# Performance work log

Measured on AMD Instinct MI355X. Metric: run time of the kernel, lower is better.

The kernel has to match this reference:

```python
import jax, jax.numpy as jnp
import numpy as np

B, S, D, E, H, K = 64, 2048, 1024, 32, 4096, 8


def setup_inputs() -> dict:
    key = jax.random.key(0)
    k0, k1, k2, k3 = jax.random.split(key, 4)
    x = jax.random.normal(k0, (B, S, D), jnp.float32)
    # gate: nn.Linear(D, E) -> weight [E, D], bias [E]
    gate_w = jax.random.normal(k1, (E, D), jnp.float32) * (1.0 / np.sqrt(D))
    gate_b = jnp.zeros((E,), jnp.float32)
    # expert weights include the bias row (input dim + 1)
    w1 = jax.random.normal(k2, (E, D + 1, H), jnp.float32) * (1.0 / np.sqrt(D + 1))
    w2 = jax.random.normal(k3, (E, H + 1, D), jnp.float32) * (1.0 / np.sqrt(H + 1))
    return {"x": x, "gate_w": gate_w, "gate_b": gate_b, "w1": w1, "w2": w2}


def reference(x, gate_w, gate_b, w1, w2):
    b, s, d = x.shape
    # gating: softmax over the TOKEN axis (expert-choice routing)
    logits = jnp.einsum('bsd,ed->bse', x, gate_w) + gate_b          # [b, s, E]
    probs = jax.nn.softmax(logits, axis=-2)                          # softmax over tokens
    # top-k tokens per expert (torch.topk over dim=-2)
    vals_t, idx_t = jax.lax.top_k(probs.transpose(0, 2, 1), K)      # [b, E, k]
    vals = vals_t.transpose(0, 2, 1)                                 # [b, k, E]
    idx = idx_t.transpose(0, 2, 1)                                   # [b, k, E]
    flat_idx = idx.reshape(b, K * E)                                 # gather order: [k, E] flattened
    # gather selected tokens
    tok = jnp.take_along_axis(x, flat_idx[:, :, None], axis=1)       # [b, k*E, d]
    tok = tok.reshape(b, K, E, d)
    # weighted merge (mux) of the k tokens per expert
    merged = jnp.einsum('bked,bke->bed', tok, vals)                  # [b, E, d]
    ones = jnp.ones(merged.shape[:-1] + (1,), merged.dtype)
    # expert FFN (bias folded into the extra weight row)
    h = jnp.einsum('bei,eih->beh', jnp.concatenate([merged, ones], -1), w1)
    h = jax.nn.gelu(h, approximate=False)                            # torch nn.GELU() = exact erf
    o = jnp.einsum('bej,ejo->beo', jnp.concatenate([h, ones], -1), w2)  # [b, E, d]
    # demux: broadcast expert output back to its k tokens, weighted, scatter-add
    out_tok = jnp.einsum('beo,bke->bkeo', o, vals).reshape(b, K * E, d)
    out = jnp.zeros_like(x).at[jnp.arange(b)[:, None], flat_idx].add(out_tok)
    return out
```

## Files before the change

kernel.cpp:

```cpp
#include <hip/hip_runtime.h>
#include <hip/hip_bf16.h>
#include <math.h>

constexpr int NB = 64;
constexpr int NS = 2048;
constexpr int ND = 1024;
constexpr int NE = 32;
constexpr int NH = 4096;
constexpr int NK = 8;

typedef short bf16x8 __attribute__((ext_vector_type(8)));
typedef float f32x4  __attribute__((ext_vector_type(4)));

__device__ __forceinline__ unsigned short f2bf_rne(float v) {
  unsigned u = __builtin_bit_cast(unsigned, v);
  u += 0x7fffu + ((u >> 16) & 1u);
  return (unsigned short)(u >> 16);
}

__device__ __forceinline__ void gload_lds16(const void* g, void* l) {
  __builtin_amdgcn_global_load_lds(
      (const __attribute__((address_space(1))) unsigned*)g,
      (__attribute__((address_space(3))) unsigned*)l, 16, 0, 0);
}

__global__ __launch_bounds__(256) void k_gate_mfma(const float* __restrict__ x,
                                                   const float* __restrict__ gw,
                                                   float* __restrict__ logitsT) {
  const int b  = blockIdx.y;
  const int s0 = blockIdx.x * 128;
  const int t  = threadIdx.x;
  const int l  = t & 63;
  const int w  = t >> 6;

  __shared__ char smem[40960];
  float* trans = (float*)smem;

  f32x4 acc[2][2] = {};

  const int xr_ = t >> 4, xc = (t & 15) * 4;
  const int ge = t >> 3,  gk = (t & 7) * 8;

  float xreg[8][4];
  float wreg[8];

  auto issue = [&](int kt) {
    const int k0 = kt * 64;
#pragma unroll
    for (int p = 0; p < 8; ++p) {
      const int r = p * 16 + xr_;
      *(float4*)xreg[p] = *(const float4*)&x[((size_t)b * NS + s0 + r) * ND + k0 + xc];
    }
    *(float4*)&wreg[0] = *(const float4*)&gw[(size_t)ge * ND + k0 + gk];
    *(float4*)&wreg[4] = *(const float4*)&gw[(size_t)ge * ND + k0 + gk + 4];
  };
  auto commit = [&](int dst) {
    short* Ah = (short*)(smem + dst * 16384);
    short* Bh = (short*)(smem + 32768 + dst * 4096);
#pragma unroll
    for (int p = 0; p < 8; ++p) {
      const int r = p * 16 + xr_;
      unsigned short h[4];
#pragma unroll
      for (int j = 0; j < 4; ++j) h[j] = f2bf_rne(xreg[p][j]);
      const int off = r * 64 + (xc ^ ((r & 7) * 8));
      *(ushort4*)&Ah[off] = *(const ushort4*)h;
    }
    unsigned short h8[8];
#pragma unroll
    for (int j = 0; j < 8; ++j) h8[j] = f2bf_rne(wreg[j]);
    const int boff = ge * 64 + (gk ^ ((ge & 7) * 8));
    *(uint4*)&Bh[boff] = *(const uint4*)h8;
  };
  auto mfma_phase = [&](int cur) {
    const short* Ah = (const short*)(smem + cur * 16384);
    const short* Bh = (const short*)(smem + 32768 + cur * 4096);
#pragma unroll
    for (int ks = 0; ks < 2; ++ks) {
      const int koff = ks * 32 + (l >> 4) * 8;
      bf16x8 a[2], bb[2];
#pragma unroll
      for (int mf = 0; mf < 2; ++mf) {
        const int r = w * 32 + mf * 16 + (l & 15);
        a[mf] = *(const bf16x8*)&Ah[r * 64 + (koff ^ ((r & 7) * 8))];
      }
#pragma unroll
      for (int nf = 0; nf < 2; ++nf) {
        const int n = nf * 16 + (l & 15);
        bb[nf] = *(const bf16x8*)&Bh[n * 64 + (koff ^ ((n & 7) * 8))];
      }
#pragma unroll
      for (int mf = 0; mf < 2; ++mf)
#pragma unroll
        for (int nf = 0; nf < 2; ++nf)
          acc[mf][nf] = __builtin_amdgcn_mfma_f32_16x16x32_bf16(a[mf], bb[nf], acc[mf][nf], 0, 0, 0);
    }
  };

  issue(0);
  commit(0);
  __syncthreads();
  int cur = 0;
  for (int kt = 0; kt < ND / 64; ++kt) {
    const bool more = (kt + 1 < ND / 64);
    if (more) issue(kt + 1);
    mfma_phase(cur);
    if (more) commit(cur ^ 1);
    __syncthreads();
    cur ^= 1;
  }

#pragma unroll
  for (int mf = 0; mf < 2; ++mf)
#pragma unroll
    for (int nf = 0; nf < 2; ++nf)
#pragma unroll
      for (int j = 0; j < 4; ++j) {
        const int sl = w * 32 + mf * 16 + (l >> 4) * 4 + j;
        const int ec = nf * 16 + (l & 15);
        trans[sl * 33 + ec] = acc[mf][nf][j];
      }
  __syncthreads();
  const int eo = t >> 3, sc = (t & 7) * 16;
#pragma unroll
  for (int j4 = 0; j4 < 4; ++j4) {
    float4 v;
    v.x = trans[(sc + j4 * 4 + 0) * 33 + eo];
    v.y = trans[(sc + j4 * 4 + 1) * 33 + eo];
    v.z = trans[(sc + j4 * 4 + 2) * 33 + eo];
    v.w = trans[(sc + j4 * 4 + 3) * 33 + eo];
    *(float4*)&logitsT[((size_t)b * NE + eo) * NS + s0 + sc + j4 * 4] = v;
  }
}

__global__ __launch_bounds__(256) void k_topk(const float* __restrict__ logitsT,
                                              const float* __restrict__ x,
                                              const float* __restrict__ gw,
                                              float* __restrict__ tval,
                                              int* __restrict__ tidx) {
  const int be = blockIdx.x, b = be >> 5, e = be & 31;
  const float* row = logitsT + (size_t)be * NS;
  const int t = threadIdx.x, w = t >> 6, lane = t & 63;

  __shared__ float  cv[64];
  __shared__ int    cix[64];
  __shared__ double wsum[4];
  __shared__ float  smax;
  __shared__ int    gci[16];
  __shared__ float  glc[16];
  __shared__ double ginv;

  float v[8]; int si[8];
#pragma unroll
  for (int j = 0; j < 8; ++j) {
    const int s = w * 512 + lane + j * 64;
    v[j] = row[s]; si[j] = s;
  }
#pragma unroll
  for (int i = 0; i < 7; ++i)
#pragma unroll
    for (int j = 0; j < 7 - i; ++j) {
      const bool sw = (v[j + 1] > v[j]) || (v[j + 1] == v[j] && si[j + 1] < si[j]);
      const float tv = sw ? v[j + 1] : v[j];
      const int   ti = sw ? si[j + 1] : si[j];
      v[j + 1] = sw ? v[j] : v[j + 1];  si[j + 1] = sw ? si[j] : si[j + 1];
      v[j] = tv;  si[j] = ti;
    }
  const float mxl = v[0];
  double s8 = 1.0;
#pragma unroll
  for (int j = 1; j < 8; ++j) s8 += (double)expf(v[j] - mxl);

  for (int r = 0; r < 16; ++r) {
    float bp = v[0]; int bi = si[0]; int bl = lane;
#pragma unroll
    for (int off = 1; off < 64; off <<= 1) {
      const float op = __shfl_xor(bp, off);
      const int   oi = __shfl_xor(bi, off);
      const int   ol = __shfl_xor(bl, off);
      if (op > bp || (op == bp && oi < bi)) { bp = op; bi = oi; bl = ol; }
    }
    if (lane == 0) { cv[w * 16 + r] = bp; cix[w * 16 + r] = bi; }
    if (lane == bl) {
      v[0]=v[1]; v[1]=v[2]; v[2]=v[3]; v[3]=v[4]; v[4]=v[5]; v[5]=v[6]; v[6]=v[7]; v[7]=-INFINITY;
      si[0]=si[1]; si[1]=si[2]; si[2]=si[3]; si[3]=si[4]; si[4]=si[5]; si[5]=si[6]; si[6]=si[7]; si[7]=0x7fffffff;
    }
  }
  __syncthreads();
  if (w == 0) {
    float mv = cv[lane]; int mi = cix[lane];
    for (int r = 0; r < 16; ++r) {
      float bp = mv; int bi = mi; int bl = lane;
#pragma unroll
      for (int off = 1; off < 64; off <<= 1) {
        const float op = __shfl_xor(bp, off);
        const int   oi = __shfl_xor(bi, off);
        const int   ol = __shfl_xor(bl, off);
        if (op > bp || (op == bp && oi < bi)) { bp = op; bi = oi; bl = ol; }
      }
      if (lane == 0) { gci[r] = bi; if (r == 0) smax = bp; }
      if (lane == bl) { mv = -INFINITY; mi = 0x7fffffff; }
    }
  }
  __syncthreads();
  const float mx = smax;
  double lsum = s8 * (double)expf(mxl - mx);
#pragma unroll
  for (int off = 32; off; off >>= 1) lsum += __shfl_xor(lsum, off);
  if (lane == 0) wsum[w] = lsum;
  __syncthreads();
  if (t == 0) ginv = 1.0 / (wsum[0] + wsum[1] + wsum[2] + wsum[3]);

  const int kb = lane * 16;
  float gwl[16];
  *(float4*)&gwl[0]  = *(const float4*)&gw[(size_t)e * ND + kb];
  *(float4*)&gwl[4]  = *(const float4*)&gw[(size_t)e * ND + kb + 4];
  *(float4*)&gwl[8]  = *(const float4*)&gw[(size_t)e * ND + kb + 8];
  *(float4*)&gwl[12] = *(const float4*)&gw[(size_t)e * ND + kb + 12];
#pragma unroll
  for (int q = 0; q < 4; ++q) {
    const int c = w * 4 + q;
    const int ciq = gci[c];
    const float* xr = x + ((size_t)b * NS + ciq) * ND + kb;
    float xv[16];
    *(float4*)&xv[0]  = *(const float4*)&xr[0];
    *(float4*)&xv[4]  = *(const float4*)&xr[4];
    *(float4*)&xv[8]  = *(const float4*)&xr[8];
    *(float4*)&xv[12] = *(const float4*)&xr[12];
    double d = 0.0;
#pragma unroll
    for (int j2 = 0; j2 < 16; ++j2) d += (double)xv[j2] * (double)gwl[j2];
#pragma unroll
    for (int off = 32; off; off >>= 1) d += __shfl_xor(d, off);
    if (lane == 0) glc[c] = (float)d;
  }
  __syncthreads();
  if (t < 16) {
    const float mylc = glc[t]; const int myci = gci[t];
    int rank = 0;
#pragma unroll
    for (int c2 = 0; c2 < 16; ++c2) {
      if (c2 == t) continue;
      rank += (glc[c2] > mylc) || (glc[c2] == mylc && gci[c2] < myci);
    }
    if (rank < 8) {
      tval[be * 8 + rank] = (float)((double)expf(mylc - mx) * ginv);
      tidx[be * 8 + rank] = myci;
    }
  }
}

__global__ __launch_bounds__(256) void k_merge(const float* __restrict__ x,
                                               const float* __restrict__ tval,
                                               const int* __restrict__ tidx,
                                               unsigned short* __restrict__ A1) {
  const int be = blockIdx.x;
  const int b  = be >> 5;
  const int e  = be & 31;
  const int t  = threadIdx.x;
  float4 acc = {0.f, 0.f, 0.f, 0.f};
#pragma unroll
  for (int k = 0; k < 8; ++k) {
    float v = tval[be * 8 + k];
    int   s = tidx[be * 8 + k];
    float4 xv = *(const float4*)&x[((size_t)b * NS + s) * ND + t * 4];
    acc.x += v * xv.x; acc.y += v * xv.y; acc.z += v * xv.z; acc.w += v * xv.w;
  }
  const int kt = t >> 4;
  const int g  = (t & 15) >> 1;
  const size_t off = ((size_t)(e * 16 + kt)) * 4096 + b * 64 + ((g ^ (b & 7)) << 3) + (t & 1) * 4;
  unsigned short h4[4] = {f2bf_rne(acc.x), f2bf_rne(acc.y), f2bf_rne(acc.z), f2bf_rne(acc.w)};
  *(ushort4*)&A1[off] = *(const ushort4*)h4;
}

template <int K, int N, bool GELU>
__global__ __launch_bounds__(256, 4) void k_ffn(const unsigned short* __restrict__ AT,
                                                const float* __restrict__ W,
                                                unsigned short* __restrict__ OT,
                                                float* __restrict__ Of) {
  constexpr int KT = K / 64;
  const int e  = blockIdx.y;
  const int n0 = blockIdx.x * 64;
  const int t  = threadIdx.x, l = t & 63, w = t >> 6;
  const int wr = w >> 1, wc = w & 1;

  __shared__ char smem[32768];

  const float* Wbase = W + (size_t)e * (K + 1) * N;
  f32x4 acc[2][2] = {};

  const int wn  = l;
  const int wk0 = w * 8;
  float wreg[2][8];

  auto issueW = [&](int kt) {
    const float* Wg = Wbase + (size_t)(kt * 64) * N + n0 + wn;
#pragma unroll
    for (int rn = 0; rn < 2; ++rn)
#pragma unroll
      for (int j = 0; j < 8; ++j)
        wreg[rn][j] = Wg[(size_t)(wk0 + rn * 32 + j) * N];
  };
  auto issueA = [&](int kt, int dst) {
    const unsigned short* at = AT + ((size_t)(e * KT + kt)) * 4096;
    char* Ab = smem + dst * 8192;
#pragma unroll
    for (int p = 0; p < 2; ++p)
      gload_lds16(at + p * 2048 + t * 8, Ab + p * 4096 + w * 1024);
  };
  auto commitW = [&](int dst) {
    short* Bb = (short*)(smem + 16384 + dst * 8192);
#pragma unroll
    for (int rn = 0; rn < 2; ++rn) {
      const int kr = (wk0 + rn * 32) >> 3;
      unsigned short s8[8];
#pragma unroll
      for (int j = 0; j < 8; ++j) s8[j] = f2bf_rne(wreg[rn][j]);
      *(uint4*)&Bb[wn * 64 + ((kr ^ (wn & 7)) << 3)] = *(const uint4*)s8;
    }
  };
  auto mfma_phase = [&](int cur) {
    const short* Ab = (const short*)(smem + cur * 8192);
    const short* Bb = (const short*)(smem + 16384 + cur * 8192);
#pragma unroll
    for (int ks = 0; ks < 2; ++ks) {
      const int g8 = ks * 4 + (l >> 4);
      bf16x8 a[2], bb[2];
#pragma unroll
      for (int mf = 0; mf < 2; ++mf) {
        const int m = wr * 32 + mf * 16 + (l & 15);
        a[mf] = *(const bf16x8*)&Ab[m * 64 + ((g8 ^ (m & 7)) << 3)];
      }
#pragma unroll
      for (int nf = 0; nf < 2; ++nf) {
        const int n = wc * 32 + nf * 16 + (l & 15);
        bb[nf] = *(const bf16x8*)&Bb[n * 64 + ((g8 ^ (n & 7)) << 3)];
      }
#pragma unroll
      for (int mf = 0; mf < 2; ++mf)
#pragma unroll
        for (int nf = 0; nf < 2; ++nf)
          acc[mf][nf] = __builtin_amdgcn_mfma_f32_16x16x32_bf16(a[mf], bb[nf], acc[mf][nf], 0, 0, 0);
    }
  };

  issueW(0); issueA(0, 0);
  commitW(0);
  __syncthreads();
  int cur = 0;
  for (int kt = 0; kt < KT; ++kt) {
    const bool more = (kt + 1 < KT);
    if (more) { issueW(kt + 1); issueA(kt + 1, cur ^ 1); }
    mfma_phase(cur);
    if (more) commitW(cur ^ 1);
    __syncthreads();
    cur ^= 1;
  }

  if (GELU) {
    unsigned short* transU = (unsigned short*)smem;
#pragma unroll
    for (int nf = 0; nf < 2; ++nf) {
      const int c = wc * 32 + nf * 16 + (l & 15);
      const float bias = Wbase[(size_t)K * N + n0 + c];
#pragma unroll
      for (int mf = 0; mf < 2; ++mf)
#pragma unroll
        for (int j = 0; j < 4; ++j) {
          const int m = wr * 32 + mf * 16 + (l >> 4) * 4 + j;
          float vv = acc[mf][nf][j] + bias;
          vv = 0.5f * vv * (1.0f + erff(vv * 0.70710678118654752440f));
          transU[m * 72 + c] = f2bf_rne(vv);
        }
    }
    __syncthreads();
    const int m  = t >> 2;
    const int c0 = (t & 3) * 16;
    const size_t tb = ((size_t)(e * (N / 64) + blockIdx.x)) * 4096;
    uint4 v0 = *(const uint4*)&transU[m * 72 + c0];
    uint4 v1 = *(const uint4*)&transU[m * 72 + c0 + 8];
    const int g0 = c0 >> 3;
    *(uint4*)&OT[tb + m * 64 + ((g0 ^ (m & 7)) << 3)]       = v0;
    *(uint4*)&OT[tb + m * 64 + (((g0 + 1) ^ (m & 7)) << 3)] = v1;
  } else {
    float* transF = (float*)smem;
#pragma unroll
    for (int nf = 0; nf < 2; ++nf) {
      const int c = wc * 32 + nf * 16 + (l & 15);
      const float bias = Wbase[(size_t)K * N + n0 + c];
#pragma unroll
      for (int mf = 0; mf < 2; ++mf)
#pragma unroll
        for (int j = 0; j < 4; ++j) {
          const int m = wr * 32 + mf * 16 + (l >> 4) * 4 + j;
          transF[m * 68 + c] = acc[mf][nf][j] + bias;
        }
    }
    __syncthreads();
    const int m  = t >> 2;
    const int c0 = (t & 3) * 16;
    float* og = Of + ((size_t)m * NE + e) * ND + n0 + c0;
    *(float4*)&og[0]  = *(const float4*)&transF[m * 68 + c0];
    *(float4*)&og[4]  = *(const float4*)&transF[m * 68 + c0 + 4];
    *(float4*)&og[8]  = *(const float4*)&transF[m * 68 + c0 + 8];
    *(float4*)&og[12] = *(const float4*)&transF[m * 68 + c0 + 12];
  }
}

__global__ __launch_bounds__(256) void k_scatter(const float* __restrict__ Obuf,
                                                 const float* __restrict__ tval,
                                                 const int* __restrict__ tidx,
                                                 float* __restrict__ out) {
  const int s0 = blockIdx.x * 8;
  const int b  = blockIdx.y;
  const int t  = threadIdx.x;
  const int w  = t >> 6;
  __shared__ unsigned long long masks[8][4];

  const int myIdx = tidx[b * 256 + t];
#pragma unroll
  for (int j = 0; j < 8; ++j) {
    unsigned long long m = __ballot(myIdx == s0 + j);
    if ((t & 63) == 0) masks[j][w] = m;
  }
  __syncthreads();

#pragma unroll
  for (int j = 0; j < 8; ++j) {
    float4 acc = {0.f, 0.f, 0.f, 0.f};
#pragma unroll
    for (int q = 0; q < 4; ++q) {
      unsigned long long mm = masks[j][q];
      while (mm) {
        int bit = __ffsll(mm) - 1;
        mm &= mm - 1;
        int r = q * 64 + bit;
        float v = tval[b * 256 + r];
        const float4 ov = *(const float4*)&Obuf[((size_t)b * NE + (r >> 3)) * ND + t * 4];
        acc.x += v * ov.x; acc.y += v * ov.y; acc.z += v * ov.z; acc.w += v * ov.w;
      }
    }
    *(float4*)&out[((size_t)b * NS + s0 + j) * ND + t * 4] = acc;
  }
}

extern "C" void kernel_launch(void* const* d_in, const int* in_sizes, int n_in,
                              void* d_out, int out_size, void* d_ws, size_t ws_size,
                              hipStream_t stream) {
  const float* x  = (const float*)d_in[0];
  const float* gw = (const float*)d_in[1];
  const float* w1 = (const float*)d_in[3];
  const float* w2 = (const float*)d_in[4];
  float* out = (float*)d_out;

  char* ws = (char*)d_ws;
  float* logitsT     = (float*)ws;
  float* tval        = (float*)(ws + 16777216);
  int*   tidx        = (int*)  (ws + 16842752);
  unsigned short* A1 = (unsigned short*)(ws + 16908288);
  unsigned short* Hb = (unsigned short*)(ws + 21102592);
  float* Obuf        = (float*)(ws + 37879808);

  k_gate_mfma<<<dim3(NS / 128, NB), 256, 0, stream>>>(x, gw, logitsT);
  k_topk<<<NB * NE, 256, 0, stream>>>(logitsT, x, gw, tval, tidx);
  k_merge<<<NB * NE, 256, 0, stream>>>(x, tval, tidx, A1);
  k_ffn<ND, NH, true ><<<dim3(NH / 64, NE), 256, 0, stream>>>(A1, w1, Hb, nullptr);
  k_ffn<NH, ND, false><<<dim3(ND / 64, NE), 256, 0, stream>>>(Hb, w2, nullptr, Obuf);
  k_scatter<<<dim3(NS / 8, NB), 256, 0, stream>>>(Obuf, tval, tidx, out);
}
```

Before: 570.9 us.

## Give each gate wave a private LDS slice and keep gate weights in registers

The gating GEMM is reorganised so that each wave loads, converts and stores only its own 32 token rows into a per-wave LDS region, while the gate-weight B fragments are loaded directly into registers in MFMA layout. This removes the shared B tile and the per-iteration block barriers, and raises register prefetch to two tiles ahead. Separately, the scatter kernel now handles 16 tokens per block instead of 8, halving the block count and the repeated tidx ballots. The risks are higher register pressure and redundant gate-weight loads across waves.

```diff
diff --git a/kernel.cpp b/kernel.cpp
--- a/kernel.cpp
+++ b/kernel.cpp
@@ -33,83 +33,84 @@
   const int l  = t & 63;
   const int w  = t >> 6;
 
-  __shared__ char smem[40960];
+  __shared__ char smem[32768];
   float* trans = (float*)smem;
 
   f32x4 acc[2][2] = {};
 
-  const int xr_ = t >> 4, xc = (t & 15) * 4;
-  const int ge = t >> 3,  gk = (t & 7) * 8;
-
-  float xreg[8][4];
-  float wreg[8];
-
-  auto issue = [&](int kt) {
-    const int k0 = kt * 64;
-#pragma unroll
-    for (int p = 0; p < 8; ++p) {
-      const int r = p * 16 + xr_;
-      *(float4*)xreg[p] = *(const float4*)&x[((size_t)b * NS + s0 + r) * ND + k0 + xc];
-    }
-    *(float4*)&wreg[0] = *(const float4*)&gw[(size_t)ge * ND + k0 + gk];
-    *(float4*)&wreg[4] = *(const float4*)&gw[(size_t)ge * ND + k0 + gk + 4];
-  };
-  auto commit = [&](int dst) {
-    short* Ah = (short*)(smem + dst * 16384);
-    short* Bh = (short*)(smem + 32768 + dst * 4096);
-#pragma unroll
-    for (int p = 0; p < 8; ++p) {
-      const int r = p * 16 + xr_;
+  const int srow = l >> 1;
+  const int scol = (l & 1) * 32;
+
+  float  xreg[8][4];
+  float  breg[4][8];
+  bf16x8 bfrag[4];
+
+  auto issueX = [&](int kt) {
+    const float* xr = &x[((size_t)b * NS + s0 + w * 32 + srow) * ND + kt * 64 + scol];
+#pragma unroll
+    for (int j = 0; j < 8; ++j) *(float4*)xreg[j] = *(const float4*)&xr[j * 4];
+  };
+  auto issueB = [&](int kt) {
+#pragma unroll
+    for (int nf = 0; nf < 2; ++nf)
+#pragma unroll
+      for (int ks = 0; ks < 2; ++ks) {
+        const float* gr = &gw[(size_t)(nf * 16 + (l & 15)) * ND + kt * 64 + ks * 32 + (l >> 4) * 8];
+        *(float4*)&breg[nf * 2 + ks][0] = *(const float4*)&gr[0];
+        *(float4*)&breg[nf * 2 + ks][4] = *(const float4*)&gr[4];
+      }
+  };
+  auto commitX = [&](int dst) {
+    short* Ah = (short*)(smem + dst * 16384 + w * 4096);
+#pragma unroll
+    for (int j = 0; j < 8; ++j) {
       unsigned short h[4];
 #pragma unroll
-      for (int j = 0; j < 4; ++j) h[j] = f2bf_rne(xreg[p][j]);
-      const int off = r * 64 + (xc ^ ((r & 7) * 8));
-      *(ushort4*)&Ah[off] = *(const ushort4*)h;
-    }
-    unsigned short h8[8];
-#pragma unroll
-    for (int j = 0; j < 8; ++j) h8[j] = f2bf_rne(wreg[j]);
-    const int boff = ge * 64 + (gk ^ ((ge & 7) * 8));
-    *(uint4*)&Bh[boff] = *(const uint4*)h8;
-  };
-  auto mfma_phase = [&](int cur) {
-    const short* Ah = (const short*)(smem + cur * 16384);
-    const short* Bh = (const short*)(smem + 32768 + cur * 4096);
+      for (int q = 0; q < 4; ++q) h[q] = f2bf_rne(xreg[j][q]);
+      const int col = scol + j * 4;
+      *(ushort4*)&Ah[srow * 64 + (col ^ ((srow & 7) * 8))] = *(const ushort4*)h;
+    }
+  };
+  auto convB = [&]() {
+#pragma unroll
+    for (int f = 0; f < 4; ++f) {
+      unsigned short h8[8];
+#pragma unroll
+      for (int j = 0; j < 8; ++j) h8[j] = f2bf_rne(breg[f][j]);
+      bfrag[f] = *(const bf16x8*)h8;
+    }
+  };
+  auto mfmaPhase = [&](int cur) {
+    const short* Ah = (const short*)(smem + cur * 16384 + w * 4096);
 #pragma unroll
     for (int ks = 0; ks < 2; ++ks) {
       const int koff = ks * 32 + (l >> 4) * 8;
-      bf16x8 a[2], bb[2];
+      bf16x8 a[2];
 #pragma unroll
       for (int mf = 0; mf < 2; ++mf) {
-        const int r = w * 32 + mf * 16 + (l & 15);
-        a[mf] = *(const bf16x8*)&Ah[r * 64 + (koff ^ ((r & 7) * 8))];
-      }
-#pragma unroll
-      for (int nf = 0; nf < 2; ++nf) {
-        const int n = nf * 16 + (l & 15);
-        bb[nf] = *(const bf16x8*)&Bh[n * 64 + (koff ^ ((n & 7) * 8))];
+        const int rl = mf * 16 + (l & 15);
+        a[mf] = *(const bf16x8*)&Ah[rl * 64 + (koff ^ ((rl & 7) * 8))];
       }
 #pragma unroll
       for (int mf = 0; mf < 2; ++mf)
 #pragma unroll
         for (int nf = 0; nf < 2; ++nf)
-          acc[mf][nf] = __builtin_amdgcn_mfma_f32_16x16x32_bf16(a[mf], bb[nf], acc[mf][nf], 0, 0, 0);
-    }
-  };
-
-  issue(0);
-  commit(0);
-  __syncthreads();
-  int cur = 0;
+          acc[mf][nf] = __builtin_amdgcn_mfma_f32_16x16x32_bf16(a[mf], bfrag[nf * 2 + ks], acc[mf][nf], 0, 0, 0);
+    }
+  };
+
+  issueX(0); issueB(0);
+  commitX(0); convB();
+  issueX(1); issueB(1);
+
+#pragma unroll 2
   for (int kt = 0; kt < ND / 64; ++kt) {
-    const bool more = (kt + 1 < ND / 64);
-    if (more) issue(kt + 1);
-    mfma_phase(cur);
-    if (more) commit(cur ^ 1);
-    __syncthreads();
-    cur ^= 1;
-  }
-
+    mfmaPhase(kt & 1);
+    if (kt + 1 < ND / 64) { commitX((kt + 1) & 1); convB(); }
+    if (kt + 2 < ND / 64) { issueX(kt + 2); issueB(kt + 2); }
+  }
+
+  __syncthreads();
 #pragma unroll
   for (int mf = 0; mf < 2; ++mf)
 #pragma unroll
@@ -411,22 +412,22 @@
                                                  const float* __restrict__ tval,
                                                  const int* __restrict__ tidx,
                                                  float* __restrict__ out) {
-  const int s0 = blockIdx.x * 8;
+  const int s0 = blockIdx.x * 16;
   const int b  = blockIdx.y;
   const int t  = threadIdx.x;
   const int w  = t >> 6;
-  __shared__ unsigned long long masks[8][4];
+  __shared__ unsigned long long masks[16][4];
 
   const int myIdx = tidx[b * 256 + t];
 #pragma unroll
-  for (int j = 0; j < 8; ++j) {
+  for (int j = 0; j < 16; ++j) {
     unsigned long long m = __ballot(myIdx == s0 + j);
     if ((t & 63) == 0) masks[j][w] = m;
   }
   __syncthreads();
 
 #pragma unroll
-  for (int j = 0; j < 8; ++j) {
+  for (int j = 0; j < 16; ++j) {
     float4 acc = {0.f, 0.f, 0.f, 0.f};
 #pragma unroll
     for (int q = 0; q < 4; ++q) {
@@ -466,5 +467,5 @@
   k_merge<<<NB * NE, 256, 0, stream>>>(x, tval, tidx, A1);
   k_ffn<ND, NH, true ><<<dim3(NH / 64, NE), 256, 0, stream>>>(A1, w1, Hb, nullptr);
   k_ffn<NH, ND, false><<<dim3(ND / 64, NE), 256, 0, stream>>>(Hb, w2, nullptr, Obuf);
-  k_scatter<<<dim3(NS / 8, NB), 256, 0, stream>>>(Obuf, tval, tidx, out);
-}
+  k_scatter<<<dim3(NS / 16, NB), 256, 0, stream>>>(Obuf, tval, tidx, out);
+}
```

Result: faster. 556.0 us (-2.6%).
